# Optimization experiments

Measured on AMD Instinct MI355X. Metric: run time of the kernel, lower is better.

The kernel has to match this reference:

```python
import jax, jax.numpy as jnp
import numpy as np

N_QUBITS = 10
N_LAYERS = 6
EMB_DIM = 64
BATCH = 16384
DIM = 2 ** N_QUBITS

# PauliZ sign table: signs[k, i] = +1 if wire i's bit in basis state k is 0 else -1
_k = np.arange(DIM)
Z_SIGNS = jnp.asarray(1 - 2 * ((_k[:, None] >> (N_QUBITS - 1 - np.arange(N_QUBITS))) & 1), dtype=jnp.float32)


def _apply_1q(state, U, wire):
    # state: [B, 2^n]; U: [2,2] (shared) or [B,2,2] (per-sample)
    B = state.shape[0]
    left = 2 ** wire
    right = DIM // (2 * left)
    st = state.reshape(B, left, 2, right)
    if U.ndim == 3:
        st = jnp.einsum('bpq,blqr->blpr', U, st)
    else:
        st = jnp.einsum('pq,blqr->blpr', U, st)
    return st.reshape(B, DIM)


def _apply_cnot(state, c, t):
    # CNOT(control=c, target=t) on the batched statevector
    B = state.shape[0]
    st = state.reshape((B,) + (2,) * N_QUBITS)
    ca, ta = c + 1, t + 1
    c0 = jnp.take(st, 0, axis=ca)
    c1 = jnp.take(st, 1, axis=ca)
    ta2 = ta - 1 if ta > ca else ta  # axis shift after take()
    c1 = jnp.flip(c1, axis=ta2)
    st = jnp.stack([c0, c1], axis=ca)
    return st.reshape(B, DIM)


def _rot_matrix(phi, theta, omega):
    # PennyLane Rot(phi, theta, omega) = RZ(omega) @ RY(theta) @ RZ(phi)
    c = jnp.cos(theta / 2)
    s = jnp.sin(theta / 2)
    return jnp.stack([
        jnp.stack([jnp.exp(-0.5j * (phi + omega)) * c, -jnp.exp(0.5j * (phi - omega)) * s]),
        jnp.stack([jnp.exp(-0.5j * (phi - omega)) * s, jnp.exp(0.5j * (phi + omega)) * c]),
    ])


def setup_inputs() -> dict:
    key = jax.random.key(0)
    k1, k2, k3 = jax.random.split(key, 3)
    x = jax.random.normal(k1, (BATCH, EMB_DIM), dtype=jnp.float32)
    W = jax.random.normal(k2, (N_QUBITS, EMB_DIM), dtype=jnp.float32) * (1.0 / np.sqrt(EMB_DIM).astype(np.float32))
    b = jnp.zeros((N_QUBITS,), dtype=jnp.float32)
    weights = jax.random.uniform(k3, (N_LAYERS, N_QUBITS, 3), dtype=jnp.float32, maxval=2.0 * np.pi)
    return {"x": x, "W": W, "b": b, "weights": weights}


def reference(x, W, b, weights):
    B = x.shape[0]
    angles = x @ W.T + b  # input projection to n_qubits angles, [B, n]
    state = jnp.zeros((B, DIM), dtype=jnp.complex64).at[:, 0].set(1.0)
    # AngleEmbedding: RX(angle_w) on each wire w (PennyLane default rotation='X')
    for w in range(N_QUBITS):
        th = angles[:, w]
        c = jnp.cos(th / 2)
        s = jnp.sin(th / 2)
        U = jnp.stack([jnp.stack([c, -1j * s], axis=-1),
                       jnp.stack([-1j * s, c], axis=-1)], axis=1)  # [B,2,2]
        state = _apply_1q(state, U, w)
    # StronglyEntanglingLayers: per layer, Rot on every wire then ring of CNOTs with range r
    for l in range(N_LAYERS):
        for w in range(N_QUBITS):
            U = _rot_matrix(weights[l, w, 0], weights[l, w, 1], weights[l, w, 2])
            state = _apply_1q(state, U, w)
        r = (l % (N_QUBITS - 1)) + 1
        for w in range(N_QUBITS):
            state = _apply_cnot(state, w, (w + r) % N_QUBITS)
    probs = jnp.real(state * jnp.conj(state))  # [B, 2^n]
    return probs @ Z_SIGNS  # PauliZ expvals, [B, n_qubits]
```

## Files before the change

### kernel.cpp

```cpp
#include <hip/hip_runtime.h>


namespace {

constexpr int NQ = 10;
constexpr int NGATES = 50;

struct Sched {
  unsigned v[NGATES];
  unsigned R[NGATES];
  unsigned Rfin[NQ];
  bool ok;
};

constexpr int par(unsigned x) { int p = 0; while (x) { p ^= 1; x &= x - 1; } return p; }

constexpr Sched make_sched() {
  Sched s{};
  unsigned cols[NQ] = {};
  unsigned rows[NQ] = {};
  for (int b = 0; b < NQ; ++b) { cols[b] = 1u << b; rows[b] = 1u << b; }
  int g = 0;
  for (int l = 0; l < 6; ++l) {
    if (l > 0) {
      for (int w = 0; w < NQ; ++w) {
        int b = 9 - w;
        s.v[g] = cols[b];
        s.R[g] = rows[b];
        ++g;
      }
    }
    int r = l % 9 + 1;
    for (int w = 0; w < NQ; ++w) {
      int c = w, t = (w + r) % NQ;
      int cb = 9 - c, tb = 9 - t;
      cols[cb] ^= cols[tb];
      rows[tb] ^= rows[cb];
    }
  }
  for (int b = 0; b < NQ; ++b) s.Rfin[b] = rows[b];
  bool ok = true;
  for (int a = 0; a < NQ; ++a)
    for (int b = 0; b < NQ; ++b)
      if (par(rows[a] & cols[b]) != (a == b ? 1 : 0)) ok = false;
  s.ok = ok;
  return s;
}

constexpr Sched SCH = make_sched();
static_assert(SCH.ok, "GF(2) schedule inconsistent");

}

__device__ float g_rots[60 * 8];

__global__ void setup_rots_kernel(const float* __restrict__ wts) {
  int idx = threadIdx.x;
  if (idx < 60) {
    float phi = wts[idx * 3 + 0], th = wts[idx * 3 + 1], om = wts[idx * 3 + 2];
    float c, sn;
    sincosf(0.5f * th, &sn, &c);
    float ca, sa, cb, sb;
    sincosf(0.5f * (phi + om), &sa, &ca);
    sincosf(0.5f * (phi - om), &sb, &cb);
    float* o = g_rots + idx * 8;
    o[0] =  ca * c;   o[1] = -sa * c;
    o[2] = -cb * sn;  o[3] = -sb * sn;
    o[4] =  cb * sn;  o[5] = -sb * sn;
    o[6] =  ca * c;   o[7] =  sa * c;
  }
}

__device__ __forceinline__ float bperm(int baddr, float v) {
  return __int_as_float(__builtin_amdgcn_ds_bpermute(baddr, __float_as_int(v)));
}

template<int M>
__device__ __forceinline__ float swz(float v) {
  return __int_as_float(__builtin_amdgcn_ds_swizzle(__float_as_int(v), (M << 10) | 0x1F));
}

typedef unsigned uint2v __attribute__((ext_vector_type(2)));

__device__ __forceinline__ float red64(float t) {
  t += swz<1>(t);  t += swz<2>(t);  t += swz<4>(t);
  t += swz<8>(t);  t += swz<16>(t);
  uint2v r = __builtin_amdgcn_permlane32_swap(__float_as_uint(t), __float_as_uint(t),
                                              false, false);
  return __uint_as_float(r.x) + __uint_as_float(r.y);
}

template<int G>
__device__ __forceinline__ void apply_gate(const float4 uA, const float4 uB,
                                           float (&ar)[16], float (&ai)[16],
                                           const int lane) {
  constexpr int v  = (int)SCH.v[G];
  constexpr int R  = (int)SCH.R[G];
  constexpr int vl = v & 15, vh = v >> 4;
  constexpr int Rl = R & 15, Rh = R >> 4;

  bool ph = false;
  if constexpr (Rh != 0) ph = (__popc(lane & Rh) & 1) != 0;
  const float dAr = ph ? uB.z : uA.x, dAi = ph ? uB.w : uA.y;
  const float oAr = ph ? uB.x : uA.z, oAi = ph ? uB.y : uA.w;
  const float dBr = ph ? uA.x : uB.z, dBi = ph ? uA.y : uB.w;
  const float oBr = ph ? uA.z : uB.x, oBi = ph ? uA.w : uB.y;

  if constexpr (vh == 0) {
#pragma unroll
    for (int i = 0; i < 16; ++i) {
      const int j = i ^ vl;
      if (j > i) {
        const bool ci = (__popc(i & Rl) & 1) != 0;
        const bool cj = (__popc(j & Rl) & 1) != 0;
        const float d0r = ci ? dBr : dAr, d0i = ci ? dBi : dAi;
        const float o0r = ci ? oBr : oAr, o0i = ci ? oBi : oAi;
        const float d1r = cj ? dBr : dAr, d1i = cj ? dBi : dAi;
        const float o1r = cj ? oBr : oAr, o1i = cj ? oBi : oAi;
        const float xr = ar[i], xi = ai[i], yr = ar[j], yi = ai[j];
        ar[i] = d0r * xr - d0i * xi + o0r * yr - o0i * yi;
        ai[i] = d0r * xi + d0i * xr + o0r * yi + o0i * yr;
        ar[j] = d1r * yr - d1i * yi + o1r * xr - o1i * xi;
        ai[j] = d1r * yi + d1i * yr + o1r * xi + o1i * xr;
      }
    }
  } else {
    int baddr = 0;
    if constexpr (vh >= 32) baddr = (lane ^ vh) << 2;
    auto fetch = [&](float x) -> float {
      if constexpr (vh < 32) return swz<vh>(x);
      else                   return bperm(baddr, x);
    };

    if constexpr (vl == 0) {
#pragma unroll
      for (int i = 0; i < 16; ++i) {
        const float pr = fetch(ar[i]);
        const float pi = fetch(ai[i]);
        const bool ci = (__popc(i & Rl) & 1) != 0;
        const float ddr = ci ? dBr : dAr, ddi = ci ? dBi : dAi;
        const float oor = ci ? oBr : oAr, ooi = ci ? oBi : oAi;
        const float xr = ar[i], xi = ai[i];
        ar[i] = ddr * xr - ddi * xi + oor * pr - ooi * pi;
        ai[i] = ddr * xi + ddi * xr + oor * pi + ooi * pr;
      }
    } else {
#pragma unroll
      for (int i = 0; i < 16; ++i) {
        const int j = i ^ vl;
        if (j > i) {
          const float qjr = fetch(ar[j]);
          const float qji = fetch(ai[j]);
          const float qir = fetch(ar[i]);
          const float qii = fetch(ai[i]);
          const bool ci = (__popc(i & Rl) & 1) != 0;
          const bool cj = (__popc(j & Rl) & 1) != 0;
          const float d0r = ci ? dBr : dAr, d0i = ci ? dBi : dAi;
          const float o0r = ci ? oBr : oAr, o0i = ci ? oBi : oAi;
          const float d1r = cj ? dBr : dAr, d1i = cj ? dBi : dAi;
          const float o1r = cj ? oBr : oAr, o1i = cj ? oBi : oAi;
          const float xr = ar[i], xi = ai[i], yr = ar[j], yi = ai[j];
          ar[i] = d0r * xr - d0i * xi + o0r * qjr - o0i * qji;
          ai[i] = d0r * xi + d0i * xr + o0r * qji + o0i * qjr;
          ar[j] = d1r * yr - d1i * yi + o1r * qir - o1i * qii;
          ai[j] = d1r * yi + d1i * yr + o1r * qii + o1i * qir;
        }
      }
    }
  }
}

template<int G>
__device__ __forceinline__ void run_gates(const float4 uA, const float4 uB,
                                          float (&ar)[16], float (&ai)[16],
                                          const int lane) {
  float4 nA, nB;
  if constexpr (G + 1 < NGATES) {
    nA = *(const float4*)(g_rots + (NQ + G + 1) * 8);
    nB = *(const float4*)(g_rots + (NQ + G + 1) * 8 + 4);
  }
  apply_gate<G>(uA, uB, ar, ai, lane);
  if constexpr (G + 1 < NGATES) run_gates<G + 1>(nA, nB, ar, ai, lane);
}

__launch_bounds__(256)
__global__ void qlayer_kernel(const float* __restrict__ x,
                              const float* __restrict__ W,
                              const float* __restrict__ bias,
                              float* __restrict__ out) {
  const int lane = threadIdx.x & 63;
  const int s = blockIdx.x * 4 + (threadIdx.x >> 6);

  const float xl = x[s * 64 + lane];
  float wl[NQ];
#pragma unroll
  for (int w = 0; w < NQ; ++w) wl[w] = W[w * 64 + lane];

  float cw[NQ], sw[NQ];
#pragma unroll
  for (int w = 0; w < NQ; ++w) {
    const float p = red64(xl * wl[w]);
    const float half = 0.5f * (p + bias[w]);
    float ss, cc;
    __sincosf(half, &ss, &cc);
    sw[w] = ss; cw[w] = cc;
  }

  float g0r[NQ], g0i[NQ], g1r[NQ], g1i[NQ];
#pragma unroll
  for (int w = 0; w < NQ; ++w) {
    const float4 uA = *(const float4*)(g_rots + w * 8);
    const float4 uB = *(const float4*)(g_rots + w * 8 + 4);
    const float c = cw[w], sn = sw[w];
    g0r[w] = uA.x * c + uA.w * sn;
    g0i[w] = uA.y * c - uA.z * sn;
    g1r[w] = uB.x * c + uB.w * sn;
    g1i[w] = uB.y * c - uB.z * sn;
  }

  float Fr, Fi;
  {
    const int b0 = (lane >> 5) & 1;
    Fr = b0 ? g1r[0] : g0r[0];
    Fi = b0 ? g1i[0] : g0i[0];
#pragma unroll
    for (int w = 1; w < 6; ++w) {
      const int bt = (lane >> (5 - w)) & 1;
      const float gr = bt ? g1r[w] : g0r[w];
      const float gi = bt ? g1i[w] : g0i[w];
      const float nr = Fr * gr - Fi * gi;
      const float ni = Fr * gi + Fi * gr;
      Fr = nr; Fi = ni;
    }
  }

  float ar[16], ai[16];
  {
    float thr[4], thi[4], tlr[4], tli[4];
#pragma unroll
    for (int a2 = 0; a2 < 4; ++a2) {
      const int bh = (a2 >> 1) & 1, bl = a2 & 1;
      {
        const float xr = bh ? g1r[6] : g0r[6], xi = bh ? g1i[6] : g0i[6];
        const float yr = bl ? g1r[7] : g0r[7], yi = bl ? g1i[7] : g0i[7];
        thr[a2] = xr * yr - xi * yi; thi[a2] = xr * yi + xi * yr;
      }
      {
        const float xr = bh ? g1r[8] : g0r[8], xi = bh ? g1i[8] : g0i[8];
        const float yr = bl ? g1r[9] : g0r[9], yi = bl ? g1i[9] : g0i[9];
        tlr[a2] = xr * yr - xi * yi; tli[a2] = xr * yi + xi * yr;
      }
    }
#pragma unroll
    for (int i = 0; i < 16; ++i) {
      const float pr = thr[i >> 2] * tlr[i & 3] - thi[i >> 2] * tli[i & 3];
      const float pi = thr[i >> 2] * tli[i & 3] + thi[i >> 2] * tlr[i & 3];
      ar[i] = Fr * pr - Fi * pi;
      ai[i] = Fr * pi + Fi * pr;
    }
  }

  {
    const float4 uA0 = *(const float4*)(g_rots + NQ * 8);
    const float4 uB0 = *(const float4*)(g_rots + NQ * 8 + 4);
    run_gates<0>(uA0, uB0, ar, ai, lane);
  }

  float pb[16];
#pragma unroll
  for (int i = 0; i < 16; ++i) pb[i] = ar[i] * ar[i] + ai[i] * ai[i];
#pragma unroll
  for (int lev = 1; lev < 16; lev <<= 1) {
#pragma unroll
    for (int i = 0; i < 16; ++i) {
      if (!(i & lev)) {
        const float A = pb[i], Bv = pb[i | lev];
        pb[i] = A + Bv;
        pb[i | lev] = A - Bv;
      }
    }
  }
#pragma unroll
  for (int q = 0; q < NQ; ++q) {
    const int R = (int)SCH.Rfin[9 - q];
    const int Rl = R & 15, Rh = R >> 4;
    float t = pb[Rl];
    if (Rh != 0) {
      const bool ph = (__popc(lane & Rh) & 1) != 0;
      t = ph ? -t : t;
    }
    t = red64(t);
    if (lane == 0) out[s * NQ + q] = t;
  }
}

extern "C" void kernel_launch(void* const* d_in, const int* in_sizes, int n_in,
                              void* d_out, int out_size, void* d_ws, size_t ws_size,
                              hipStream_t stream) {
  const float* x   = (const float*)d_in[0];
  const float* W   = (const float*)d_in[1];
  const float* b   = (const float*)d_in[2];
  const float* wts = (const float*)d_in[3];
  float* out = (float*)d_out;
  const int B = in_sizes[0] / 64;

  setup_rots_kernel<<<1, 64, 0, stream>>>(wts);
  qlayer_kernel<<<B / 4, 256, 0, stream>>>(x, W, b, out);
}
```

Baseline: 250.6 us.

## Fuse rotation setup into main kernel via shared memory and use explicit FMAs

Removes the separate single-block setup kernel. Each block now computes the 60 rotation matrices into shared memory and synchronises before using them, and gate coefficients are read from LDS instead of global memory. Complex multiply-adds are also rewritten as explicit fmaf chains so they contract to FMA instructions. The cost is redundant trig work in every block (4096 blocks), plus a barrier and some LDS traffic.

```diff
diff --git a/kernel.cpp b/kernel.cpp
--- a/kernel.cpp
+++ b/kernel.cpp
@@ -52,39 +52,20 @@
 
 }
 
-__device__ float g_rots[60 * 8];
-
-__global__ void setup_rots_kernel(const float* __restrict__ wts) {
-  int idx = threadIdx.x;
-  if (idx < 60) {
-    float phi = wts[idx * 3 + 0], th = wts[idx * 3 + 1], om = wts[idx * 3 + 2];
-    float c, sn;
-    sincosf(0.5f * th, &sn, &c);
-    float ca, sa, cb, sb;
-    sincosf(0.5f * (phi + om), &sa, &ca);
-    sincosf(0.5f * (phi - om), &sb, &cb);
-    float* o = g_rots + idx * 8;
-    o[0] =  ca * c;   o[1] = -sa * c;
-    o[2] = -cb * sn;  o[3] = -sb * sn;
-    o[4] =  cb * sn;  o[5] = -sb * sn;
-    o[6] =  ca * c;   o[7] =  sa * c;
-  }
-}
-
-__device__ __forceinline__ float bperm(int baddr, float v) {
+__device__ __forceinline__ float bperm1(int baddr, float v) {
   return __int_as_float(__builtin_amdgcn_ds_bpermute(baddr, __float_as_int(v)));
 }
 
 template<int M>
-__device__ __forceinline__ float swz(float v) {
+__device__ __forceinline__ float swz1(float v) {
   return __int_as_float(__builtin_amdgcn_ds_swizzle(__float_as_int(v), (M << 10) | 0x1F));
 }
 
 typedef unsigned uint2v __attribute__((ext_vector_type(2)));
 
 __device__ __forceinline__ float red64(float t) {
-  t += swz<1>(t);  t += swz<2>(t);  t += swz<4>(t);
-  t += swz<8>(t);  t += swz<16>(t);
+  t += swz1<1>(t);  t += swz1<2>(t);  t += swz1<4>(t);
+  t += swz1<8>(t);  t += swz1<16>(t);
   uint2v r = __builtin_amdgcn_permlane32_swap(__float_as_uint(t), __float_as_uint(t),
                                               false, false);
   return __uint_as_float(r.x) + __uint_as_float(r.y);
@@ -118,18 +99,18 @@
         const float d1r = cj ? dBr : dAr, d1i = cj ? dBi : dAi;
         const float o1r = cj ? oBr : oAr, o1i = cj ? oBi : oAi;
         const float xr = ar[i], xi = ai[i], yr = ar[j], yi = ai[j];
-        ar[i] = d0r * xr - d0i * xi + o0r * yr - o0i * yi;
-        ai[i] = d0r * xi + d0i * xr + o0r * yi + o0i * yr;
-        ar[j] = d1r * yr - d1i * yi + o1r * xr - o1i * xi;
-        ai[j] = d1r * yi + d1i * yr + o1r * xi + o1i * xr;
+        ar[i] = fmaf(-o0i, yi, fmaf(o0r, yr, fmaf(-d0i, xi, d0r * xr)));
+        ai[i] = fmaf( o0i, yr, fmaf(o0r, yi, fmaf( d0i, xr, d0r * xi)));
+        ar[j] = fmaf(-o1i, xi, fmaf(o1r, xr, fmaf(-d1i, yi, d1r * yr)));
+        ai[j] = fmaf( o1i, xr, fmaf(o1r, xi, fmaf( d1i, yr, d1r * yi)));
       }
     }
   } else {
     int baddr = 0;
     if constexpr (vh >= 32) baddr = (lane ^ vh) << 2;
     auto fetch = [&](float x) -> float {
-      if constexpr (vh < 32) return swz<vh>(x);
-      else                   return bperm(baddr, x);
+      if constexpr (vh < 32) return swz1<vh>(x);
+      else                   return bperm1(baddr, x);
     };
 
     if constexpr (vl == 0) {
@@ -141,8 +122,8 @@
         const float ddr = ci ? dBr : dAr, ddi = ci ? dBi : dAi;
         const float oor = ci ? oBr : oAr, ooi = ci ? oBi : oAi;
         const float xr = ar[i], xi = ai[i];
-        ar[i] = ddr * xr - ddi * xi + oor * pr - ooi * pi;
-        ai[i] = ddr * xi + ddi * xr + oor * pi + ooi * pr;
+        ar[i] = fmaf(-ooi, pi, fmaf(oor, pr, fmaf(-ddi, xi, ddr * xr)));
+        ai[i] = fmaf( ooi, pr, fmaf(oor, pi, fmaf( ddi, xr, ddr * xi)));
       }
     } else {
 #pragma unroll
@@ -160,10 +141,10 @@
           const float d1r = cj ? dBr : dAr, d1i = cj ? dBi : dAi;
           const float o1r = cj ? oBr : oAr, o1i = cj ? oBi : oAi;
           const float xr = ar[i], xi = ai[i], yr = ar[j], yi = ai[j];
-          ar[i] = d0r * xr - d0i * xi + o0r * qjr - o0i * qji;
-          ai[i] = d0r * xi + d0i * xr + o0r * qji + o0i * qjr;
-          ar[j] = d1r * yr - d1i * yi + o1r * qir - o1i * qii;
-          ai[j] = d1r * yi + d1i * yr + o1r * qii + o1i * qir;
+          ar[i] = fmaf(-o0i, qji, fmaf(o0r, qjr, fmaf(-d0i, xi, d0r * xr)));
+          ai[i] = fmaf( o0i, qjr, fmaf(o0r, qji, fmaf( d0i, xr, d0r * xi)));
+          ar[j] = fmaf(-o1i, qii, fmaf(o1r, qir, fmaf(-d1i, yi, d1r * yr)));
+          ai[j] = fmaf( o1i, qir, fmaf(o1r, qii, fmaf( d1i, yr, d1r * yi)));
         }
       }
     }
@@ -172,24 +153,43 @@
 
 template<int G>
 __device__ __forceinline__ void run_gates(const float4 uA, const float4 uB,
+                                          const float* rots_s,
                                           float (&ar)[16], float (&ai)[16],
                                           const int lane) {
   float4 nA, nB;
   if constexpr (G + 1 < NGATES) {
-    nA = *(const float4*)(g_rots + (NQ + G + 1) * 8);
-    nB = *(const float4*)(g_rots + (NQ + G + 1) * 8 + 4);
+    nA = *(const float4*)(rots_s + (NQ + G + 1) * 8);
+    nB = *(const float4*)(rots_s + (NQ + G + 1) * 8 + 4);
   }
   apply_gate<G>(uA, uB, ar, ai, lane);
-  if constexpr (G + 1 < NGATES) run_gates<G + 1>(nA, nB, ar, ai, lane);
+  if constexpr (G + 1 < NGATES) run_gates<G + 1>(nA, nB, rots_s, ar, ai, lane);
 }
 
 __launch_bounds__(256)
 __global__ void qlayer_kernel(const float* __restrict__ x,
                               const float* __restrict__ W,
                               const float* __restrict__ bias,
+                              const float* __restrict__ wts,
                               float* __restrict__ out) {
-  const int lane = threadIdx.x & 63;
-  const int s = blockIdx.x * 4 + (threadIdx.x >> 6);
+  __shared__ float rots_s[60 * 8];
+
+  const int tid  = threadIdx.x;
+  const int lane = tid & 63;
+  const int s = blockIdx.x * 4 + (tid >> 6);
+
+  if (tid < 60) {
+    const float phi = wts[tid * 3 + 0], th = wts[tid * 3 + 1], om = wts[tid * 3 + 2];
+    float c, sn;
+    sincosf(0.5f * th, &sn, &c);
+    float ca, sa, cb, sb;
+    sincosf(0.5f * (phi + om), &sa, &ca);
+    sincosf(0.5f * (phi - om), &sb, &cb);
+    float* o = rots_s + tid * 8;
+    o[0] =  ca * c;   o[1] = -sa * c;
+    o[2] = -cb * sn;  o[3] = -sb * sn;
+    o[4] =  cb * sn;  o[5] = -sb * sn;
+    o[6] =  ca * c;   o[7] =  sa * c;
+  }
 
   const float xl = x[s * 64 + lane];
   float wl[NQ];
@@ -206,16 +206,18 @@
     sw[w] = ss; cw[w] = cc;
   }
 
+  __syncthreads();
+
   float g0r[NQ], g0i[NQ], g1r[NQ], g1i[NQ];
 #pragma unroll
   for (int w = 0; w < NQ; ++w) {
-    const float4 uA = *(const float4*)(g_rots + w * 8);
-    const float4 uB = *(const float4*)(g_rots + w * 8 + 4);
+    const float4 uA = *(const float4*)(rots_s + w * 8);
+    const float4 uB = *(const float4*)(rots_s + w * 8 + 4);
     const float c = cw[w], sn = sw[w];
-    g0r[w] = uA.x * c + uA.w * sn;
-    g0i[w] = uA.y * c - uA.z * sn;
-    g1r[w] = uB.x * c + uB.w * sn;
-    g1i[w] = uB.y * c - uB.z * sn;
+    g0r[w] = fmaf(uA.w, sn, uA.x * c);
+    g0i[w] = fmaf(-uA.z, sn, uA.y * c);
+    g1r[w] = fmaf(uB.w, sn, uB.x * c);
+    g1i[w] = fmaf(-uB.z, sn, uB.y * c);
   }
 
   float Fr, Fi;
@@ -228,8 +230,8 @@
       const int bt = (lane >> (5 - w)) & 1;
       const float gr = bt ? g1r[w] : g0r[w];
       const float gi = bt ? g1i[w] : g0i[w];
-      const float nr = Fr * gr - Fi * gi;
-      const float ni = Fr * gi + Fi * gr;
+      const float nr = fmaf(-Fi, gi, Fr * gr);
+      const float ni = fmaf( Fi, gr, Fr * gi);
       Fr = nr; Fi = ni;
     }
   }
@@ -243,32 +245,32 @@
       {
         const float xr = bh ? g1r[6] : g0r[6], xi = bh ? g1i[6] : g0i[6];
         const float yr = bl ? g1r[7] : g0r[7], yi = bl ? g1i[7] : g0i[7];
-        thr[a2] = xr * yr - xi * yi; thi[a2] = xr * yi + xi * yr;
+        thr[a2] = fmaf(-xi, yi, xr * yr); thi[a2] = fmaf(xi, yr, xr * yi);
       }
       {
         const float xr = bh ? g1r[8] : g0r[8], xi = bh ? g1i[8] : g0i[8];
         const float yr = bl ? g1r[9] : g0r[9], yi = bl ? g1i[9] : g0i[9];
-        tlr[a2] = xr * yr - xi * yi; tli[a2] = xr * yi + xi * yr;
+        tlr[a2] = fmaf(-xi, yi, xr * yr); tli[a2] = fmaf(xi, yr, xr * yi);
       }
     }
 #pragma unroll
     for (int i = 0; i < 16; ++i) {
-      const float pr = thr[i >> 2] * tlr[i & 3] - thi[i >> 2] * tli[i & 3];
-      const float pi = thr[i >> 2] * tli[i & 3] + thi[i >> 2] * tlr[i & 3];
-      ar[i] = Fr * pr - Fi * pi;
-      ai[i] = Fr * pi + Fi * pr;
+      const float pr = fmaf(-thi[i >> 2], tli[i & 3], thr[i >> 2] * tlr[i & 3]);
+      const float pi = fmaf( thi[i >> 2], tlr[i & 3], thr[i >> 2] * tli[i & 3]);
+      ar[i] = fmaf(-Fi, pi, Fr * pr);
+      ai[i] = fmaf( Fi, pr, Fr * pi);
     }
   }
 
   {
-    const float4 uA0 = *(const float4*)(g_rots + NQ * 8);
-    const float4 uB0 = *(const float4*)(g_rots + NQ * 8 + 4);
-    run_gates<0>(uA0, uB0, ar, ai, lane);
+    const float4 uA0 = *(const float4*)(rots_s + NQ * 8);
+    const float4 uB0 = *(const float4*)(rots_s + NQ * 8 + 4);
+    run_gates<0>(uA0, uB0, rots_s, ar, ai, lane);
   }
 
   float pb[16];
 #pragma unroll
-  for (int i = 0; i < 16; ++i) pb[i] = ar[i] * ar[i] + ai[i] * ai[i];
+  for (int i = 0; i < 16; ++i) pb[i] = fmaf(ai[i], ai[i], ar[i] * ar[i]);
 #pragma unroll
   for (int lev = 1; lev < 16; lev <<= 1) {
 #pragma unroll
@@ -304,6 +306,5 @@
   float* out = (float*)d_out;
   const int B = in_sizes[0] / 64;
 
-  setup_rots_kernel<<<1, 64, 0, stream>>>(wts);
-  qlayer_kernel<<<B / 4, 256, 0, stream>>>(x, W, b, out);
-}
+  qlayer_kernel<<<B / 4, 256, 0, stream>>>(x, W, b, wts, out);
+}
```

Result: no change. 252.5 us (+0.8%).
